# Performance work log

Measured on AMD Instinct MI355X. Metric: run time of the kernel, lower is better.

The kernel has to match this reference:

```python
import jax, jax.numpy as jnp
import numpy as np

B, TQ, TV, D = 8, 2048, 2048, 128
NEG = 1e9  # keras Attention uses additive -1e9 masking for fp32


def setup_inputs() -> dict:
    key = jax.random.key(0)
    kq, kv, kk, kmq, kmv = jax.random.split(key, 5)
    q = jax.random.normal(kq, (B, TQ, D), dtype=jnp.float32)
    v = jax.random.normal(kv, (B, TV, D), dtype=jnp.float32)
    k = jax.random.normal(kk, (B, TV, D), dtype=jnp.float32)
    # learned scalar scale from use_scale=True, initialized to ones
    scale = jnp.ones((), dtype=jnp.float32)
    mask_q = jax.random.randint(kmq, (B, TQ), 0, 2) > 0
    mask_v = jax.random.randint(kmv, (B, TV), 0, 2) > 0
    return {"q": q, "v": v, "k": k, "scale": scale, "mask_q": mask_q, "mask_v": mask_v}


def reference(q, v, k, scale, mask_q, mask_v):
    # scores: [B, Tq, Tv]
    scores = scale * jnp.einsum('bqd,bkd->bqk', q, k)
    # key/value mask: additive -1e9 on masked positions (keras semantics)
    scores = scores - NEG * (1.0 - mask_v[:, None, :].astype(scores.dtype))
    weights = jax.nn.softmax(scores, axis=-1)
    out = jnp.einsum('bqk,bkd->bqd', weights, v)
    # query mask zeroes out masked query rows
    out = out * mask_q[:, :, None].astype(out.dtype)
    return out
```

## Files before the change

### kernel.cpp

```cpp
#include <hip/hip_runtime.h>
#include <cstddef>

#define NB 8
#define TQ 2048
#define TV 2048
#define DD 128
#define KVT 32
#define NWV 4
#define CHW (TV / NWV)
#define NT  (CHW / KVT)
#define LOG2E 1.4426950408889634f

typedef _Float16 f16x8 __attribute__((ext_vector_type(8)));
typedef _Float16 f16x4 __attribute__((ext_vector_type(4)));
typedef float f32x4 __attribute__((ext_vector_type(4)));

__device__ __forceinline__ float fast_exp2(float x) {
  return __builtin_amdgcn_exp2f(x);
}

template <int CTRL>
__device__ __forceinline__ float dpp_mov(float x) {
  return __builtin_bit_cast(float,
      __builtin_amdgcn_update_dpp(0, __builtin_bit_cast(int, x), CTRL, 0xF, 0xF, true));
}
__device__ __forceinline__ float rowmax16(float x) {
  x = fmaxf(x, dpp_mov<0x128>(x));
  x = fmaxf(x, dpp_mov<0x124>(x));
  x = fmaxf(x, dpp_mov<0x122>(x));
  x = fmaxf(x, dpp_mov<0x121>(x));
  return x;
}

__global__ __launch_bounds__(256) void prepass_kernel(
    const float* __restrict__ k, const float* __restrict__ v,
    _Float16* __restrict__ kh2, _Float16* __restrict__ vt2)
{
  __shared__ _Float16 tlds[32 * 34];
  const int tid = threadIdx.x;
  const int bid = blockIdx.x;
  if (bid < 512) {
    int b = bid >> 6, kt = bid & 63;
    int row = tid >> 3, d0 = (tid & 7) * 4;
    const float* src = k + ((size_t)(b * TV + kt * 32 + row)) * DD;
    _Float16* dst = kh2 + ((size_t)(b * 64 + kt)) * 4096;
#pragma unroll
    for (int it = 0; it < 4; ++it) {
      float4 x = *(const float4*)(src + it * 32 + d0);
      f16x4 h; h[0] = (_Float16)x.x; h[1] = (_Float16)x.y;
      h[2] = (_Float16)x.z; h[3] = (_Float16)x.w;
      *(f16x4*)(dst + it * 1024 + row * 32 + d0) = h;
    }
  } else {
    int tb = bid - 512;
    int b = tb >> 8, rem = tb & 255;
    int kt = rem >> 2, dt = rem & 3;
    int r = tid >> 3, c0 = (tid & 7) * 4;
    float4 x = *(const float4*)&v[((size_t)b * TV + kt * 32 + r) * DD + dt * 32 + c0];
    tlds[(c0 + 0) * 34 + r] = (_Float16)x.x;
    tlds[(c0 + 1) * 34 + r] = (_Float16)x.y;
    tlds[(c0 + 2) * 34 + r] = (_Float16)x.z;
    tlds[(c0 + 3) * 34 + r] = (_Float16)x.w;
    __syncthreads();
    int dl = tid >> 3, k0 = (tid & 7) * 4;
    f16x4 h;
#pragma unroll
    for (int i = 0; i < 4; ++i) h[i] = tlds[dl * 34 + k0 + i];
    size_t eidx = (((size_t)b * 64 + kt) * 128 + (dt * 32 + dl)) * 32 + k0;
    *(f16x4*)&vt2[eidx] = h;
  }
}

__global__ __launch_bounds__(256, 2) void attn_main(
    const float* __restrict__ q, const float* __restrict__ scale_p,
    const _Float16* __restrict__ kh2, const _Float16* __restrict__ vt2,
    const int* __restrict__ mask_q, const int* __restrict__ mask_v,
    float* __restrict__ out)
{
  __shared__ __align__(16) _Float16 plds_all[NWV][2][16 * 40];
  __shared__ __align__(16) float osh[32 * 132];
  __shared__ float msh[NWV][32], lsh[NWV][32];

  const int tid = threadIdx.x;
  const int w = tid >> 6;
  const int lane = tid & 63;
  const int l15 = lane & 15, lg = lane >> 4;

  const int b = blockIdx.x & 7;
  const int qg = blockIdx.x >> 3;
  const int qbase = qg * 32;
  const int kv0 = w * CHW;

  const _Float16* ktiles = kh2 + (size_t)b * 64 * 4096;
  const _Float16* vtiles = vt2 + (size_t)b * 64 * 4096;
  const int* mvb = mask_v + b * TV;

  const float sc2 = scale_p[0] * LOG2E;
  f16x8 qf[2][4];
#pragma unroll
  for (int rb = 0; rb < 2; ++rb)
#pragma unroll
    for (int kc = 0; kc < 4; ++kc) {
      const float* qp = q + ((size_t)b * TQ + qbase + rb * 16 + l15) * DD + kc * 32 + lg * 8;
      float4 xa = *(const float4*)qp;
      float4 xb = *(const float4*)(qp + 4);
      f16x8 h;
      h[0] = (_Float16)(sc2 * xa.x); h[1] = (_Float16)(sc2 * xa.y);
      h[2] = (_Float16)(sc2 * xa.z); h[3] = (_Float16)(sc2 * xa.w);
      h[4] = (_Float16)(sc2 * xb.x); h[5] = (_Float16)(sc2 * xb.y);
      h[6] = (_Float16)(sc2 * xb.z); h[7] = (_Float16)(sc2 * xb.w);
      qf[rb][kc] = h;
    }

  const unsigned short HBIAS = __builtin_bit_cast(unsigned short, (_Float16)(-60000.0f));
  unsigned mbp[NT];
#pragma unroll
  for (int t = 0; t < NT; ++t) {
    unsigned h0 = (mvb[kv0 + t * KVT + l15]      != 0) ? 0u : (unsigned)HBIAS;
    unsigned h1 = (mvb[kv0 + t * KVT + 16 + l15] != 0) ? 0u : (unsigned)HBIAS;
    mbp[t] = h0 | (h1 << 16);
  }

  f16x8 vones;
#pragma unroll
  for (int j = 0; j < 8; ++j) vones[j] = (_Float16)1.f;

  f32x4 acc[2][8];
  f32x4 accl[2];
#pragma unroll
  for (int rb = 0; rb < 2; ++rb) {
    accl[rb] = (f32x4){0.f, 0.f, 0.f, 0.f};
#pragma unroll
    for (int ct = 0; ct < 8; ++ct) acc[rb][ct] = (f32x4){0.f, 0.f, 0.f, 0.f};
  }
  float m[2][4];
#pragma unroll
  for (int rb = 0; rb < 2; ++rb)
#pragma unroll
    for (int r = 0; r < 4; ++r) m[rb][r] = -3.0e38f;

  const int tbase = w * NT;

  f16x8 kbuf[8], vbuf[8];
  {
    const _Float16* ktb = ktiles + (size_t)tbase * 4096;
#pragma unroll
    for (int kc = 0; kc < 4; ++kc) {
      kbuf[2 * kc]     = *(const f16x8*)(ktb + kc * 1024 + l15 * 32 + lg * 8);
      kbuf[2 * kc + 1] = *(const f16x8*)(ktb + kc * 1024 + (16 + l15) * 32 + lg * 8);
    }
    const _Float16* vtb = vtiles + (size_t)tbase * 4096;
#pragma unroll
    for (int ct = 0; ct < 8; ++ct)
      vbuf[ct] = *(const f16x8*)(vtb + (ct * 16 + l15) * 32 + lg * 8);
  }

#pragma unroll
  for (int t = 0; t < NT; ++t) {
    const int tile = tbase + t;

    f32x4 s[2][2];
    s[0][0] = (f32x4){0,0,0,0}; s[0][1] = (f32x4){0,0,0,0};
    s[1][0] = (f32x4){0,0,0,0}; s[1][1] = (f32x4){0,0,0,0};
    __builtin_amdgcn_s_setprio(1);
#pragma unroll
    for (int kc = 0; kc < 4; ++kc) {
      s[0][0] = __builtin_amdgcn_mfma_f32_16x16x32_f16(qf[0][kc], kbuf[2*kc],   s[0][0], 0, 0, 0);
      s[1][0] = __builtin_amdgcn_mfma_f32_16x16x32_f16(qf[1][kc], kbuf[2*kc],   s[1][0], 0, 0, 0);
      s[0][1] = __builtin_amdgcn_mfma_f32_16x16x32_f16(qf[0][kc], kbuf[2*kc+1], s[0][1], 0, 0, 0);
      s[1][1] = __builtin_amdgcn_mfma_f32_16x16x32_f16(qf[1][kc], kbuf[2*kc+1], s[1][1], 0, 0, 0);
    }
    __builtin_amdgcn_s_setprio(0);

    if (t + 1 < NT) {
      const _Float16* ktb = ktiles + (size_t)(tile + 1) * 4096;
#pragma unroll
      for (int kc = 0; kc < 4; ++kc) {
        kbuf[2 * kc]     = *(const f16x8*)(ktb + kc * 1024 + l15 * 32 + lg * 8);
        kbuf[2 * kc + 1] = *(const f16x8*)(ktb + kc * 1024 + (16 + l15) * 32 + lg * 8);
      }
    }

    const float b0 = (float)__builtin_bit_cast(_Float16, (unsigned short)(mbp[t] & 0xFFFFu));
    const float b1 = (float)__builtin_bit_cast(_Float16, (unsigned short)(mbp[t] >> 16));
    f16x8 pa[2];
#pragma unroll
    for (int rb = 0; rb < 2; ++rb) {
      float plm[4];
      bool grow = false;
#pragma unroll
      for (int r = 0; r < 4; ++r) {
        s[rb][0][r] += b0;
        s[rb][1][r] += b1;
        plm[r] = fmaxf(s[rb][0][r], s[rb][1][r]);
        grow = grow || (plm[r] > m[rb][r] + 11.5f);
      }
      if (__any(grow)) {
        f32x4 alv;
#pragma unroll
        for (int r = 0; r < 4; ++r) {
          float pmx = rowmax16(plm[r]);
          float mn = fmaxf(m[rb][r], pmx);
          alv[r] = fast_exp2(m[rb][r] - mn);
          m[rb][r] = mn;
        }
        accl[rb] *= alv;
#pragma unroll
        for (int ct = 0; ct < 8; ++ct) acc[rb][ct] *= alv;
      }
      _Float16* pl = plds_all[w][rb];
#pragma unroll
      for (int r = 0; r < 4; ++r) {
        float p0 = fast_exp2(s[rb][0][r] - m[rb][r]);
        float p1 = fast_exp2(s[rb][1][r] - m[rb][r]);
        int row = lg * 4 + r;
        pl[row * 40 + l15]      = (_Float16)p0;
        pl[row * 40 + 16 + l15] = (_Float16)p1;
      }
      pa[rb] = *(const f16x8*)(pl + l15 * 40 + lg * 8);
    }

    __builtin_amdgcn_s_setprio(1);
#pragma unroll
    for (int ct = 0; ct < 8; ++ct) {
      acc[0][ct] = __builtin_amdgcn_mfma_f32_16x16x32_f16(pa[0], vbuf[ct], acc[0][ct], 0, 0, 0);
      acc[1][ct] = __builtin_amdgcn_mfma_f32_16x16x32_f16(pa[1], vbuf[ct], acc[1][ct], 0, 0, 0);
    }
    accl[0] = __builtin_amdgcn_mfma_f32_16x16x32_f16(pa[0], vones, accl[0], 0, 0, 0);
    accl[1] = __builtin_amdgcn_mfma_f32_16x16x32_f16(pa[1], vones, accl[1], 0, 0, 0);
    __builtin_amdgcn_s_setprio(0);

    if (t + 1 < NT) {
      const _Float16* vtb = vtiles + (size_t)(tile + 1) * 4096;
#pragma unroll
      for (int ct = 0; ct < 8; ++ct)
        vbuf[ct] = *(const f16x8*)(vtb + (ct * 16 + l15) * 32 + lg * 8);
    }
  }

  if (l15 == 0) {
#pragma unroll
    for (int rb = 0; rb < 2; ++rb)
#pragma unroll
      for (int r = 0; r < 4; ++r) {
        msh[w][rb * 16 + lg * 4 + r] = m[rb][r];
        lsh[w][rb * 16 + lg * 4 + r] = accl[rb][r];
      }
  }
  __syncthreads();

  float coef[2][4];
#pragma unroll
  for (int rb = 0; rb < 2; ++rb)
#pragma unroll
    for (int r = 0; r < 4; ++r) {
      int row = rb * 16 + lg * 4 + r;
      float mstar = msh[0][row];
#pragma unroll
      for (int wv = 1; wv < NWV; ++wv) mstar = fmaxf(mstar, msh[wv][row]);
      coef[rb][r] = fast_exp2(m[rb][r] - mstar);
    }

#pragma unroll
  for (int wv = 0; wv < NWV; ++wv) {
    if (w == wv) {
#pragma unroll
      for (int rb = 0; rb < 2; ++rb)
#pragma unroll
        for (int ct = 0; ct < 8; ++ct)
#pragma unroll
          for (int r = 0; r < 4; ++r) {
            int idx = (rb * 16 + lg * 4 + r) * 132 + ct * 16 + l15;
            float val = coef[rb][r] * acc[rb][ct][r];
            if (wv == 0) osh[idx] = val; else osh[idx] += val;
          }
    }
    __syncthreads();
  }

  {
    const int row = tid >> 3;
    const int cg = (tid & 7) * 16;
    float mstar = msh[0][row];
#pragma unroll
    for (int wv = 1; wv < NWV; ++wv) mstar = fmaxf(mstar, msh[wv][row]);
    float lstar = 0.f;
#pragma unroll
    for (int wv = 0; wv < NWV; ++wv)
      lstar += fast_exp2(msh[wv][row] - mstar) * lsh[wv][row];
    const int qr = qbase + row;
    const float f = ((mask_q[(size_t)b * TQ + qr] != 0) ? 1.f : 0.f) / lstar;
    float* orow = out + ((size_t)b * TQ + qr) * DD + cg;
#pragma unroll
    for (int i4 = 0; i4 < 4; ++i4) {
      float4 p = *(float4*)&osh[row * 132 + cg + i4 * 4];
      float4 o; o.x = p.x * f; o.y = p.y * f; o.z = p.z * f; o.w = p.w * f;
      *(float4*)(orow + i4 * 4) = o;
    }
  }
}

__global__ __launch_bounds__(64, 4) void attn_f32_kernel(
    const float* __restrict__ q, const float* __restrict__ v,
    const float* __restrict__ k, const float* __restrict__ scale_p,
    const int* __restrict__ mask_q, const int* __restrict__ mask_v,
    float* __restrict__ out)
{
  __shared__ __align__(16) _Float16 plds[16 * 40];
  const int lane = threadIdx.x & 63;
  const int l15 = lane & 15, lg = lane >> 4;
  const int qblocks = TQ / 16;
  const int b = blockIdx.x / qblocks, qb = blockIdx.x % qblocks;
  const int qbase = qb * 16;
  const float scale = scale_p[0];
  const float* qp = q + ((size_t)b * TQ + qbase) * DD;
  const float* kbase = k + (size_t)b * TV * DD;
  const float* vbase = v + (size_t)b * TV * DD;
  const int* mvb = mask_v + b * TV;
  f16x8 qf[4];
#pragma unroll
  for (int kc = 0; kc < 4; ++kc) {
    float4 a = *(const float4*)(qp + (size_t)l15 * DD + kc * 32 + lg * 8);
    float4 bb = *(const float4*)(qp + (size_t)l15 * DD + kc * 32 + lg * 8 + 4);
    f16x8 h; h[0]=(_Float16)a.x;h[1]=(_Float16)a.y;h[2]=(_Float16)a.z;h[3]=(_Float16)a.w;
    h[4]=(_Float16)bb.x;h[5]=(_Float16)bb.y;h[6]=(_Float16)bb.z;h[7]=(_Float16)bb.w;
    qf[kc]=h;
  }
  f32x4 acc[8];
#pragma unroll
  for (int i = 0; i < 8; ++i) acc[i] = (f32x4){0.f,0.f,0.f,0.f};
  float m[4], lsum[4];
#pragma unroll
  for (int r = 0; r < 4; ++r) { m[r] = -3.0e38f; lsum[r] = 0.f; }
  for (int kt = 0; kt < TV; kt += KVT) {
    f32x4 s0 = {0,0,0,0}, s1 = {0,0,0,0};
#pragma unroll
    for (int kc = 0; kc < 4; ++kc) {
      const float* kp0 = kbase + (size_t)(kt + l15) * DD + kc * 32 + lg * 8;
      float4 a = *(const float4*)kp0; float4 bb = *(const float4*)(kp0 + 4);
      f16x8 kf0; kf0[0]=(_Float16)a.x;kf0[1]=(_Float16)a.y;kf0[2]=(_Float16)a.z;kf0[3]=(_Float16)a.w;
      kf0[4]=(_Float16)bb.x;kf0[5]=(_Float16)bb.y;kf0[6]=(_Float16)bb.z;kf0[7]=(_Float16)bb.w;
      s0 = __builtin_amdgcn_mfma_f32_16x16x32_f16(qf[kc], kf0, s0, 0, 0, 0);
      const float* kp1 = kbase + (size_t)(kt + 16 + l15) * DD + kc * 32 + lg * 8;
      a = *(const float4*)kp1; bb = *(const float4*)(kp1 + 4);
      f16x8 kf1; kf1[0]=(_Float16)a.x;kf1[1]=(_Float16)a.y;kf1[2]=(_Float16)a.z;kf1[3]=(_Float16)a.w;
      kf1[4]=(_Float16)bb.x;kf1[5]=(_Float16)bb.y;kf1[6]=(_Float16)bb.z;kf1[7]=(_Float16)bb.w;
      s1 = __builtin_amdgcn_mfma_f32_16x16x32_f16(qf[kc], kf1, s1, 0, 0, 0);
    }
    const float a0 = (mvb[kt + l15] != 0) ? 0.f : -1e9f;
    const float a1 = (mvb[kt + 16 + l15] != 0) ? 0.f : -1e9f;
    float pmx[4];
#pragma unroll
    for (int r = 0; r < 4; ++r) {
      s0[r] = s0[r] * scale + a0; s1[r] = s1[r] * scale + a1;
      pmx[r] = fmaxf(s0[r], s1[r]);
    }
#pragma unroll
    for (int off = 1; off < 16; off <<= 1)
#pragma unroll
      for (int r = 0; r < 4; ++r) pmx[r] = fmaxf(pmx[r], __shfl_xor(pmx[r], off, 64));
    float al[4], ps[4];
#pragma unroll
    for (int r = 0; r < 4; ++r) {
      float mn = fmaxf(m[r], pmx[r]);
      al[r] = __expf(m[r] - mn); m[r] = mn;
      float p0 = __expf(s0[r] - mn), p1 = __expf(s1[r] - mn);
      ps[r] = p0 + p1;
      int row = lg * 4 + r;
      plds[row * 40 + l15] = (_Float16)p0;
      plds[row * 40 + 16 + l15] = (_Float16)p1;
    }
#pragma unroll
    for (int off = 1; off < 16; off <<= 1)
#pragma unroll
      for (int r = 0; r < 4; ++r) ps[r] += __shfl_xor(ps[r], off, 64);
#pragma unroll
    for (int r = 0; r < 4; ++r) {
      lsum[r] = lsum[r] * al[r] + ps[r];
#pragma unroll
      for (int ct = 0; ct < 8; ++ct) acc[ct][r] *= al[r];
    }
    f16x8 pa = *(const f16x8*)&plds[l15 * 40 + lg * 8];
#pragma unroll
    for (int ct = 0; ct < 8; ++ct) {
      const float* vp = vbase + (size_t)(kt + lg * 8) * DD + ct * 16 + l15;
      f16x8 vfx;
#pragma unroll
      for (int j = 0; j < 8; ++j) vfx[j] = (_Float16)vp[(size_t)j * DD];
      acc[ct] = __builtin_amdgcn_mfma_f32_16x16x32_f16(pa, vfx, acc[ct], 0, 0, 0);
    }
  }
  const int* mqb = mask_q + b * TQ;
#pragma unroll
  for (int r = 0; r < 4; ++r) {
    int row = lg * 4 + r;
    int qr = qbase + row;
    float f = ((mqb[qr] != 0) ? 1.f : 0.f) / lsum[r];
    float* orow = out + ((size_t)b * TQ + qr) * DD;
#pragma unroll
    for (int ct = 0; ct < 8; ++ct) orow[ct * 16 + l15] = acc[ct][r] * f;
  }
}

extern "C" void kernel_launch(void* const* d_in, const int* in_sizes, int n_in,
                              void* d_out, int out_size, void* d_ws, size_t ws_size,
                              hipStream_t stream) {
  const float* q      = (const float*)d_in[0];
  const float* v      = (const float*)d_in[1];
  const float* k      = (const float*)d_in[2];
  const float* scale  = (const float*)d_in[3];
  const int*   mask_q = (const int*)d_in[4];
  const int*   mask_v = (const int*)d_in[5];
  float* out = (float*)d_out;

  const size_t need = 2ull * NB * TV * DD * sizeof(_Float16);
  if (ws_size >= need) {
    _Float16* kh2 = (_Float16*)d_ws;
    _Float16* vt2 = kh2 + (size_t)NB * TV * DD;
    hipLaunchKernelGGL(prepass_kernel, dim3(512 + 2048), dim3(256), 0, stream,
                       k, v, kh2, vt2);
    hipLaunchKernelGGL(attn_main, dim3(NB * (TQ / 32)), dim3(256), 0, stream,
                       q, scale, kh2, vt2, mask_q, mask_v, out);
  } else {
    hipLaunchKernelGGL(attn_f32_kernel, dim3(NB * (TQ / 16)), dim3(64), 0, stream,
                       q, v, k, scale, mask_q, mask_v, out);
  }
}
```

Before: 56.38 us.

## Compute transposed scores S^T to keep P in registers and drop LDS round-trip

```diff
diff --git a/kernel.cpp b/kernel.cpp
--- a/kernel.cpp
+++ b/kernel.cpp
@@ -19,22 +19,11 @@
   return __builtin_amdgcn_exp2f(x);
 }
 
-template <int CTRL>
-__device__ __forceinline__ float dpp_mov(float x) {
-  return __builtin_bit_cast(float,
-      __builtin_amdgcn_update_dpp(0, __builtin_bit_cast(int, x), CTRL, 0xF, 0xF, true));
-}
-__device__ __forceinline__ float rowmax16(float x) {
-  x = fmaxf(x, dpp_mov<0x128>(x));
-  x = fmaxf(x, dpp_mov<0x124>(x));
-  x = fmaxf(x, dpp_mov<0x122>(x));
-  x = fmaxf(x, dpp_mov<0x121>(x));
-  return x;
-}
-
 __global__ __launch_bounds__(256) void prepass_kernel(
     const float* __restrict__ k, const float* __restrict__ v,
-    _Float16* __restrict__ kh2, _Float16* __restrict__ vt2)
+    const int* __restrict__ mask_v,
+    _Float16* __restrict__ kh2, _Float16* __restrict__ vt2,
+    _Float16* __restrict__ indb)
 {
   __shared__ _Float16 tlds[32 * 34];
   const int tid = threadIdx.x;
@@ -42,6 +31,7 @@
   if (bid < 512) {
     int b = bid >> 6, kt = bid & 63;
     int row = tid >> 3, d0 = (tid & 7) * 4;
+    int R = 16 * ((row >> 2) & 1) + 4 * (row >> 3) + (row & 3);
     const float* src = k + ((size_t)(b * TV + kt * 32 + row)) * DD;
     _Float16* dst = kh2 + ((size_t)(b * 64 + kt)) * 4096;
 #pragma unroll
@@ -49,18 +39,19 @@
       float4 x = *(const float4*)(src + it * 32 + d0);
       f16x4 h; h[0] = (_Float16)x.x; h[1] = (_Float16)x.y;
       h[2] = (_Float16)x.z; h[3] = (_Float16)x.w;
-      *(f16x4*)(dst + it * 1024 + row * 32 + d0) = h;
-    }
-  } else {
+      *(f16x4*)(dst + it * 1024 + R * 32 + d0) = h;
+    }
+  } else if (bid < 512 + 2048) {
     int tb = bid - 512;
     int b = tb >> 8, rem = tb & 255;
     int kt = rem >> 2, dt = rem & 3;
     int r = tid >> 3, c0 = (tid & 7) * 4;
+    float mfac = (mask_v[(size_t)b * TV + kt * 32 + r] != 0) ? 1.f : 0.f;
     float4 x = *(const float4*)&v[((size_t)b * TV + kt * 32 + r) * DD + dt * 32 + c0];
-    tlds[(c0 + 0) * 34 + r] = (_Float16)x.x;
-    tlds[(c0 + 1) * 34 + r] = (_Float16)x.y;
-    tlds[(c0 + 2) * 34 + r] = (_Float16)x.z;
-    tlds[(c0 + 3) * 34 + r] = (_Float16)x.w;
+    tlds[(c0 + 0) * 34 + r] = (_Float16)(mfac * x.x);
+    tlds[(c0 + 1) * 34 + r] = (_Float16)(mfac * x.y);
+    tlds[(c0 + 2) * 34 + r] = (_Float16)(mfac * x.z);
+    tlds[(c0 + 3) * 34 + r] = (_Float16)(mfac * x.w);
     __syncthreads();
     int dl = tid >> 3, k0 = (tid & 7) * 4;
     f16x4 h;
@@ -68,16 +59,21 @@
     for (int i = 0; i < 4; ++i) h[i] = tlds[dl * 34 + k0 + i];
     size_t eidx = (((size_t)b * 64 + kt) * 128 + (dt * 32 + dl)) * 32 + k0;
     *(f16x4*)&vt2[eidx] = h;
+  } else {
+    int bid2 = bid - 512 - 2048;
+    size_t base = (size_t)bid2 * 1024 + tid * 4;
+#pragma unroll
+    for (int i = 0; i < 4; ++i)
+      indb[base + i] = (mask_v[base + i] != 0) ? (_Float16)1.f : (_Float16)0.f;
   }
 }
 
 __global__ __launch_bounds__(256, 2) void attn_main(
     const float* __restrict__ q, const float* __restrict__ scale_p,
     const _Float16* __restrict__ kh2, const _Float16* __restrict__ vt2,
-    const int* __restrict__ mask_q, const int* __restrict__ mask_v,
-    float* __restrict__ out)
+    const _Float16* __restrict__ indb,
+    const int* __restrict__ mask_q, float* __restrict__ out)
 {
-  __shared__ __align__(16) _Float16 plds_all[NWV][2][16 * 40];
   __shared__ __align__(16) float osh[32 * 132];
   __shared__ float msh[NWV][32], lsh[NWV][32];
 
@@ -89,11 +85,10 @@
   const int b = blockIdx.x & 7;
   const int qg = blockIdx.x >> 3;
   const int qbase = qg * 32;
-  const int kv0 = w * CHW;
 
   const _Float16* ktiles = kh2 + (size_t)b * 64 * 4096;
   const _Float16* vtiles = vt2 + (size_t)b * 64 * 4096;
-  const int* mvb = mask_v + b * TV;
+  const _Float16* indbt = indb + (size_t)b * TV;
 
   const float sc2 = scale_p[0] * LOG2E;
   f16x8 qf[2][4];
@@ -112,19 +107,6 @@
       qf[rb][kc] = h;
     }
 
-  const unsigned short HBIAS = __builtin_bit_cast(unsigned short, (_Float16)(-60000.0f));
-  unsigned mbp[NT];
-#pragma unroll
-  for (int t = 0; t < NT; ++t) {
-    unsigned h0 = (mvb[kv0 + t * KVT + l15]      != 0) ? 0u : (unsigned)HBIAS;
-    unsigned h1 = (mvb[kv0 + t * KVT + 16 + l15] != 0) ? 0u : (unsigned)HBIAS;
-    mbp[t] = h0 | (h1 << 16);
-  }
-
-  f16x8 vones;
-#pragma unroll
-  for (int j = 0; j < 8; ++j) vones[j] = (_Float16)1.f;
-
   f32x4 acc[2][8];
   f32x4 accl[2];
 #pragma unroll
@@ -133,31 +115,16 @@
 #pragma unroll
     for (int ct = 0; ct < 8; ++ct) acc[rb][ct] = (f32x4){0.f, 0.f, 0.f, 0.f};
   }
-  float m[2][4];
-#pragma unroll
-  for (int rb = 0; rb < 2; ++rb)
-#pragma unroll
-    for (int r = 0; r < 4; ++r) m[rb][r] = -3.0e38f;
+  float m[2];
+  m[0] = -3.0e38f; m[1] = -3.0e38f;
 
   const int tbase = w * NT;
-
-  f16x8 kbuf[8], vbuf[8];
-  {
-    const _Float16* ktb = ktiles + (size_t)tbase * 4096;
-#pragma unroll
-    for (int kc = 0; kc < 4; ++kc) {
-      kbuf[2 * kc]     = *(const f16x8*)(ktb + kc * 1024 + l15 * 32 + lg * 8);
-      kbuf[2 * kc + 1] = *(const f16x8*)(ktb + kc * 1024 + (16 + l15) * 32 + lg * 8);
-    }
-    const _Float16* vtb = vtiles + (size_t)tbase * 4096;
-#pragma unroll
-    for (int ct = 0; ct < 8; ++ct)
-      vbuf[ct] = *(const f16x8*)(vtb + (ct * 16 + l15) * 32 + lg * 8);
-  }
 
 #pragma unroll
   for (int t = 0; t < NT; ++t) {
     const int tile = tbase + t;
+    const _Float16* ktb = ktiles + (size_t)tile * 4096;
+    const _Float16* vtb = vtiles + (size_t)tile * 4096;
 
     f32x4 s[2][2];
     s[0][0] = (f32x4){0,0,0,0}; s[0][1] = (f32x4){0,0,0,0};
@@ -165,87 +132,82 @@
     __builtin_amdgcn_s_setprio(1);
 #pragma unroll
     for (int kc = 0; kc < 4; ++kc) {
-      s[0][0] = __builtin_amdgcn_mfma_f32_16x16x32_f16(qf[0][kc], kbuf[2*kc],   s[0][0], 0, 0, 0);
-      s[1][0] = __builtin_amdgcn_mfma_f32_16x16x32_f16(qf[1][kc], kbuf[2*kc],   s[1][0], 0, 0, 0);
-      s[0][1] = __builtin_amdgcn_mfma_f32_16x16x32_f16(qf[0][kc], kbuf[2*kc+1], s[0][1], 0, 0, 0);
-      s[1][1] = __builtin_amdgcn_mfma_f32_16x16x32_f16(qf[1][kc], kbuf[2*kc+1], s[1][1], 0, 0, 0);
+      f16x8 kf0 = *(const f16x8*)(ktb + kc * 1024 + l15 * 32 + lg * 8);
+      f16x8 kf1 = *(const f16x8*)(ktb + kc * 1024 + (16 + l15) * 32 + lg * 8);
+      s[0][0] = __builtin_amdgcn_mfma_f32_16x16x32_f16(kf0, qf[0][kc], s[0][0], 0, 0, 0);
+      s[0][1] = __builtin_amdgcn_mfma_f32_16x16x32_f16(kf0, qf[1][kc], s[0][1], 0, 0, 0);
+      s[1][0] = __builtin_amdgcn_mfma_f32_16x16x32_f16(kf1, qf[0][kc], s[1][0], 0, 0, 0);
+      s[1][1] = __builtin_amdgcn_mfma_f32_16x16x32_f16(kf1, qf[1][kc], s[1][1], 0, 0, 0);
     }
     __builtin_amdgcn_s_setprio(0);
 
-    if (t + 1 < NT) {
-      const _Float16* ktb = ktiles + (size_t)(tile + 1) * 4096;
-#pragma unroll
-      for (int kc = 0; kc < 4; ++kc) {
-        kbuf[2 * kc]     = *(const f16x8*)(ktb + kc * 1024 + l15 * 32 + lg * 8);
-        kbuf[2 * kc + 1] = *(const f16x8*)(ktb + kc * 1024 + (16 + l15) * 32 + lg * 8);
+    f16x8 indf = *(const f16x8*)(indbt + tile * 32 + lg * 8);
+    f16x8 vf[8];
+#pragma unroll
+    for (int ct = 0; ct < 8; ++ct)
+      vf[ct] = *(const f16x8*)(vtb + (ct * 16 + l15) * 32 + lg * 8);
+
+    float bias[8];
+#pragma unroll
+    for (int j = 0; j < 8; ++j) bias[j] = ((float)indf[j] - 1.f) * 60000.f;
+
+    f16x8 pa[2];
+#pragma unroll
+    for (int rb = 0; rb < 2; ++rb) {
+#pragma unroll
+      for (int r = 0; r < 4; ++r) {
+        s[0][rb][r] += bias[r];
+        s[1][rb][r] += bias[4 + r];
       }
-    }
-
-    const float b0 = (float)__builtin_bit_cast(_Float16, (unsigned short)(mbp[t] & 0xFFFFu));
-    const float b1 = (float)__builtin_bit_cast(_Float16, (unsigned short)(mbp[t] >> 16));
-    f16x8 pa[2];
-#pragma unroll
-    for (int rb = 0; rb < 2; ++rb) {
-      float plm[4];
-      bool grow = false;
-#pragma unroll
-      for (int r = 0; r < 4; ++r) {
-        s[rb][0][r] += b0;
-        s[rb][1][r] += b1;
-        plm[r] = fmaxf(s[rb][0][r], s[rb][1][r]);
-        grow = grow || (plm[r] > m[rb][r] + 11.5f);
-      }
-      if (__any(grow)) {
+      float pm = fmaxf(fmaxf(fmaxf(s[0][rb][0], s[0][rb][1]), fmaxf(s[0][rb][2], s[0][rb][3])),
+                       fmaxf(fmaxf(s[1][rb][0], s[1][rb][1]), fmaxf(s[1][rb][2], s[1][rb][3])));
+      pm = fmaxf(pm, __shfl_xor(pm, 16, 64));
+      pm = fmaxf(pm, __shfl_xor(pm, 32, 64));
+      if (__any(pm > m[rb] + 11.5f)) {
+        float mn = fmaxf(m[rb], pm);
+        float alpha = fast_exp2(m[rb] - mn);
+        m[rb] = mn;
         f32x4 alv;
 #pragma unroll
-        for (int r = 0; r < 4; ++r) {
-          float pmx = rowmax16(plm[r]);
-          float mn = fmaxf(m[rb][r], pmx);
-          alv[r] = fast_exp2(m[rb][r] - mn);
-          m[rb][r] = mn;
-        }
+        for (int r = 0; r < 4; ++r)
+          alv[r] = __shfl(alpha, lg * 4 + r, 64);
         accl[rb] *= alv;
 #pragma unroll
         for (int ct = 0; ct < 8; ++ct) acc[rb][ct] *= alv;
       }
-      _Float16* pl = plds_all[w][rb];
-#pragma unroll
-      for (int r = 0; r < 4; ++r) {
-        float p0 = fast_exp2(s[rb][0][r] - m[rb][r]);
-        float p1 = fast_exp2(s[rb][1][r] - m[rb][r]);
-        int row = lg * 4 + r;
-        pl[row * 40 + l15]      = (_Float16)p0;
-        pl[row * 40 + 16 + l15] = (_Float16)p1;
-      }
-      pa[rb] = *(const f16x8*)(pl + l15 * 40 + lg * 8);
+      f16x8 p;
+      p[0] = (_Float16)fast_exp2(s[0][rb][0] - m[rb]);
+      p[1] = (_Float16)fast_exp2(s[0][rb][1] - m[rb]);
+      p[2] = (_Float16)fast_exp2(s[0][rb][2] - m[rb]);
+      p[3] = (_Float16)fast_exp2(s[0][rb][3] - m[rb]);
+      p[4] = (_Float16)fast_exp2(s[1][rb][0] - m[rb]);
+      p[5] = (_Float16)fast_exp2(s[1][rb][1] - m[rb]);
+      p[6] = (_Float16)fast_exp2(s[1][rb][2] - m[rb]);
+      p[7] = (_Float16)fast_exp2(s[1][rb][3] - m[rb]);
+      pa[rb] = p;
     }
 
     __builtin_amdgcn_s_setprio(1);
 #pragma unroll
     for (int ct = 0; ct < 8; ++ct) {
-      acc[0][ct] = __builtin_amdgcn_mfma_f32_16x16x32_f16(pa[0], vbuf[ct], acc[0][ct], 0, 0, 0);
-      acc[1][ct] = __builtin_amdgcn_mfma_f32_16x16x32_f16(pa[1], vbuf[ct], acc[1][ct], 0, 0, 0);
-    }
-    accl[0] = __builtin_amdgcn_mfma_f32_16x16x32_f16(pa[0], vones, accl[0], 0, 0, 0);
-    accl[1] = __builtin_amdgcn_mfma_f32_16x16x32_f16(pa[1], vones, accl[1], 0, 0, 0);
+      acc[0][ct] = __builtin_amdgcn_mfma_f32_16x16x32_f16(pa[0], vf[ct], acc[0][ct], 0, 0, 0);
+      acc[1][ct] = __builtin_amdgcn_mfma_f32_16x16x32_f16(pa[1], vf[ct], acc[1][ct], 0, 0, 0);
+    }
+    accl[0] = __builtin_amdgcn_mfma_f32_16x16x32_f16(pa[0], indf, accl[0], 0, 0, 0);
+    accl[1] = __builtin_amdgcn_mfma_f32_16x16x32_f16(pa[1], indf, accl[1], 0, 0, 0);
     __builtin_amdgcn_s_setprio(0);
-
-    if (t + 1 < NT) {
-      const _Float16* vtb = vtiles + (size_t)(tile + 1) * 4096;
-#pragma unroll
-      for (int ct = 0; ct < 8; ++ct)
-        vbuf[ct] = *(const f16x8*)(vtb + (ct * 16 + l15) * 32 + lg * 8);
-    }
-  }
-
+  }
+
+  if (lg == 0) {
+    msh[w][l15]      = m[0];
+    msh[w][16 + l15] = m[1];
+  }
   if (l15 == 0) {
 #pragma unroll
     for (int rb = 0; rb < 2; ++rb)
 #pragma unroll
-      for (int r = 0; r < 4; ++r) {
-        msh[w][rb * 16 + lg * 4 + r] = m[rb][r];
+      for (int r = 0; r < 4; ++r)
         lsh[w][rb * 16 + lg * 4 + r] = accl[rb][r];
-      }
   }
   __syncthreads();
 
@@ -258,7 +220,7 @@
       float mstar = msh[0][row];
 #pragma unroll
       for (int wv = 1; wv < NWV; ++wv) mstar = fmaxf(mstar, msh[wv][row]);
-      coef[rb][r] = fast_exp2(m[rb][r] - mstar);
+      coef[rb][r] = fast_exp2(msh[w][row] - mstar);
     }
 
 #pragma unroll
@@ -413,14 +375,16 @@
   const int*   mask_v = (const int*)d_in[5];
   float* out = (float*)d_out;
 
-  const size_t need = 2ull * NB * TV * DD * sizeof(_Float16);
-  if (ws_size >= need) {
+  const size_t kvBytes = 2ull * NB * TV * DD * sizeof(_Float16);
+  const size_t indBytes = (size_t)NB * TV * sizeof(_Float16);
+  if (ws_size >= kvBytes + indBytes) {
     _Float16* kh2 = (_Float16*)d_ws;
     _Float16* vt2 = kh2 + (size_t)NB * TV * DD;
-    hipLaunchKernelGGL(prepass_kernel, dim3(512 + 2048), dim3(256), 0, stream,
-                       k, v, kh2, vt2);
+    _Float16* indb = vt2 + (size_t)NB * TV * DD;
+    hipLaunchKernelGGL(prepass_kernel, dim3(512 + 2048 + 16), dim3(256), 0, stream,
+                       k, v, mask_v, kh2, vt2, indb);
     hipLaunchKernelGGL(attn_main, dim3(NB * (TQ / 32)), dim3(256), 0, stream,
-                       q, scale, kh2, vt2, mask_q, mask_v, out);
+                       q, scale, kh2, vt2, indb, mask_q, out);
   } else {
     hipLaunchKernelGGL(attn_f32_kernel, dim3(NB * (TQ / 16)), dim3(64), 0, stream,
                        q, v, k, scale, mask_q, mask_v, out);
```

Result: faster. 53.74 us (-4.7%).
